# Kernel optimization log

Measured on AMD Instinct MI355X. Metric: run time of the kernel, lower is better.

## Reference

```python
import jax, jax.numpy as jnp
import numpy as np
import math

DIM = 1024
NUM_HEADS = 16
HEAD_DIM = DIM // NUM_HEADS
WINDOW = 256


def setup_inputs() -> dict:
    key = jax.random.key(0)
    k1, k2, k3 = jax.random.split(key, 3)
    B, T = 2, 2048
    x = jax.random.normal(k1, (B, T, DIM), dtype=jnp.float32)
    # nn.Linear weights: [out, in]; y = x @ W.T
    w_qkv = jax.random.normal(k2, (3 * DIM, DIM), dtype=jnp.float32) * (1.0 / math.sqrt(DIM))
    w_out = jax.random.normal(k3, (DIM, DIM), dtype=jnp.float32) * (1.0 / math.sqrt(DIM))
    return {"x": x, "w_qkv": w_qkv, "w_out": w_out}


def _apply_rotary(x, cos, sin):
    # x: [B,H,T,D]; cos/sin: [T, D//2] broadcast over B,H
    d = x.shape[-1] // 2
    x1, x2 = x[..., :d], x[..., d:]
    return jnp.concatenate([x1 * cos - x2 * sin, x2 * cos + x1 * sin], axis=-1)


def reference(x, w_qkv, w_out):
    B, T, C = x.shape
    H, Dh = NUM_HEADS, HEAD_DIM
    qkv = (x @ w_qkv.T).reshape(B, T, 3, H, Dh)
    q, k, v = qkv[:, :, 0], qkv[:, :, 1], qkv[:, :, 2]  # [B,T,H,Dh]
    q = jnp.transpose(q, (0, 2, 1, 3))  # [B,H,T,Dh]
    k = jnp.transpose(k, (0, 2, 1, 3))
    v = jnp.transpose(v, (0, 2, 1, 3))
    # RoPE tables
    inv_freq = 1.0 / (10000.0 ** (jnp.arange(0, Dh, 2, dtype=jnp.float32) / Dh))
    t = jnp.arange(T, dtype=jnp.float32)
    freqs = jnp.einsum('i,j->ij', t, inv_freq)  # [T, Dh//2]
    cos, sin = jnp.cos(freqs), jnp.sin(freqs)
    q = _apply_rotary(q, cos, sin)
    k = _apply_rotary(k, cos, sin)
    scale = 1.0 / math.sqrt(Dh)
    attn = jnp.einsum('bhqd,bhkd->bhqk', q, k) * scale  # [B,H,T,T]
    i = jnp.arange(T)[:, None]
    j = jnp.arange(T)[None, :]
    allowed = (j <= i) & ((i - j) < WINDOW)  # causal + sliding window
    attn = jnp.where(allowed, attn, -jnp.inf)
    attn = jax.nn.softmax(attn, axis=-1)
    out = jnp.einsum('bhqk,bhkd->bhqd', attn, v)
    out = jnp.transpose(out, (0, 2, 1, 3)).reshape(B, T, C)
    return out @ w_out.T
```

## Files before the change

### kernel.cpp

```cpp
#include <hip/hip_runtime.h>
#include <stdint.h>
#include <math.h>

#define T_SEQ 2048
#define NHEAD 16
#define WIN 256

typedef unsigned short u16;
typedef __attribute__((ext_vector_type(8))) short short8;
typedef __attribute__((ext_vector_type(4))) float f32x4;

typedef const __attribute__((address_space(1))) void* gas_ptr;
typedef __attribute__((address_space(3))) void* las_ptr;

__device__ __forceinline__ u16 f2bf(float f) {
  uint32_t u = __builtin_bit_cast(uint32_t, f);
  u += 0x7fffu + ((u >> 16) & 1u);
  return (u16)(u >> 16);
}
__device__ __forceinline__ float bf2f(u16 v) {
  return __builtin_bit_cast(float, ((uint32_t)v) << 16);
}
__device__ __forceinline__ void g2l16(const u16* g, u16* l) {
  __builtin_amdgcn_global_load_lds((gas_ptr)g, (las_ptr)l, 16, 0, 0);
}

__global__ __launch_bounds__(256) void cast_bf16_k(const float* __restrict__ in,
                                                   u16* __restrict__ out, int n4) {
  int i = blockIdx.x * 256 + threadIdx.x;
  if (i >= n4) return;
  const float4 v = reinterpret_cast<const float4*>(in)[i];
  union { u16 h[4]; uint64_t q; } o;
  o.h[0] = f2bf(v.x); o.h[1] = f2bf(v.y); o.h[2] = f2bf(v.z); o.h[3] = f2bf(v.w);
  reinterpret_cast<uint64_t*>(out)[i] = o.q;
}

template <int MODE, typename OUT_T>
__global__ __launch_bounds__(256) void gemm_nt(const u16* __restrict__ A,
                                               const u16* __restrict__ B,
                                               OUT_T* __restrict__ C,
                                               u16* __restrict__ Qb,
                                               u16* __restrict__ Kb,
                                               u16* __restrict__ Vt,
                                               int M, int N, int K) {
  __shared__ u16 lA[3][4096];
  __shared__ u16 lB[3][4096];
  const int tid = threadIdx.x;
  const int lane = tid & 63;
  const int wave = tid >> 6;
  const int r = lane & 15, g = lane >> 4;
  const int wr = wave >> 1, wc = wave & 1;

  const int nbn = N >> 7;
  const int bnpx = nbn >> 3;
  const int bid = blockIdx.x;
  const int xcd = bid & 7, ii = bid >> 3;
  const int bn = xcd * bnpx + (ii % bnpx);
  const int bm = ii / bnpx;

  const u16* Abase = A + (size_t)bm * 128 * K;
  const u16* Bbase = B + (size_t)bn * 128 * K;

  f32x4 acc[4][4];
#pragma unroll
  for (int m = 0; m < 4; m++)
#pragma unroll
    for (int n = 0; n < 4; n++) acc[m][n] = (f32x4){0.f, 0.f, 0.f, 0.f};

  const int c0 = tid, c1 = 256 + tid;
  const int row0 = c0 >> 2, row1 = c1 >> 2;
  const int sw0 = ((c0 & 3) ^ (row0 & 3)) * 8;
  const int sw1 = ((c1 & 3) ^ (row1 & 3)) * 8;
  const int ldsb = wave * 512;

  auto stage = [&](int k0, int b) {
    g2l16(Abase + (size_t)row0 * K + k0 + sw0, &lA[b][ldsb]);
    g2l16(Abase + (size_t)row1 * K + k0 + sw1, &lA[b][2048 + ldsb]);
    g2l16(Bbase + (size_t)row0 * K + k0 + sw0, &lB[b][ldsb]);
    g2l16(Bbase + (size_t)row1 * K + k0 + sw1, &lB[b][2048 + ldsb]);
  };

  const int nt = K >> 5;
  stage(0, 0);
  if (nt > 1) stage(32, 1);
  int cur = 0, pre = 2;

  const int rsw = (r & 3);
  for (int t = 0; t < nt; ++t) {
    if (t + 1 < nt) asm volatile("s_waitcnt vmcnt(4)" ::: "memory");
    else            asm volatile("s_waitcnt vmcnt(0)" ::: "memory");
    __builtin_amdgcn_s_barrier();
    if (t + 2 < nt) stage((t + 2) * 32, pre);

    const u16* la = lA[cur];
    const u16* lb = lB[cur];
    short8 af[4], bfr[4];
#pragma unroll
    for (int m = 0; m < 4; m++)
      af[m] = *reinterpret_cast<const short8*>(
          &la[(wr * 64 + m * 16 + r) * 32 + ((g ^ rsw) * 8)]);
#pragma unroll
    for (int n = 0; n < 4; n++)
      bfr[n] = *reinterpret_cast<const short8*>(
          &lb[(wc * 64 + n * 16 + r) * 32 + ((g ^ rsw) * 8)]);
#pragma unroll
    for (int m = 0; m < 4; m++)
#pragma unroll
      for (int n = 0; n < 4; n++)
        acc[m][n] = __builtin_amdgcn_mfma_f32_16x16x32_bf16(af[m], bfr[n], acc[m][n], 0, 0, 0);
    asm volatile("s_waitcnt lgkmcnt(0)" ::: "memory");
    cur = (cur == 2) ? 0 : cur + 1;
    pre = (pre == 2) ? 0 : pre + 1;
  }

  if constexpr (MODE == 0) {
#pragma unroll
    for (int m = 0; m < 4; m++) {
      const int row = bm * 128 + wr * 64 + m * 16 + g * 4;
#pragma unroll
      for (int n = 0; n < 4; n++) {
        const int col = bn * 128 + wc * 64 + n * 16 + r;
#pragma unroll
        for (int j = 0; j < 4; j++) {
          float v = acc[m][n][j];
          if constexpr (sizeof(OUT_T) == 2)
            C[(size_t)(row + j) * N + col] = f2bf(v);
          else
            C[(size_t)(row + j) * N + col] = v;
        }
      }
    }
  } else {
    const int reg = bn >> 3;
    const int b = bm >> 4;
    const int h = ((bn & 7) << 1) + wc;
    const int bh = b * NHEAD + h;
    const int t0 = ((bm & 15) << 7) + wr * 64;

    if (reg == 2) {
      u16* vb = Vt + (size_t)bh * 64 * T_SEQ;
#pragma unroll
      for (int n = 0; n < 4; n++) {
        const int d = n * 16 + r;
#pragma unroll
        for (int m = 0; m < 4; m++) {
          const int t = t0 + m * 16 + g * 4;
#pragma unroll
          for (int j = 0; j < 4; j++)
            vb[(size_t)d * T_SEQ + t + j] = f2bf(acc[m][n][j]);
        }
      }
    } else {
      u16* qk = (reg == 0 ? Qb : Kb) + (size_t)bh * T_SEQ * 64;
#pragma unroll
      for (int n = 0; n < 2; n++) {
        const int d = n * 16 + r;
        const float inv = exp2f(-(float)d * 0.41524101186092029f);
#pragma unroll
        for (int m = 0; m < 4; m++) {
          const int tb = t0 + m * 16 + g * 4;
#pragma unroll
          for (int j = 0; j < 4; j++) {
            const int t = tb + j;
            float s, c;
            __sincosf((float)t * inv, &s, &c);
            const float x1 = acc[m][n][j], x2 = acc[m][n + 2][j];
            qk[(size_t)t * 64 + d]      = f2bf(x1 * c - x2 * s);
            qk[(size_t)t * 64 + d + 32] = f2bf(x2 * c + x1 * s);
          }
        }
      }
    }
  }
}

__device__ __forceinline__ void stage_kv(const u16* __restrict__ Kh,
                                         const u16* __restrict__ Vh, int k0,
                                         u16* lk, u16* lv, int tid) {
  const int wave = tid >> 6;
#pragma unroll
  for (int p = 0; p < 2; p++) {
    int c = p * 256 + tid;
    int row = c >> 3;
    int col = ((c & 7) ^ (row & 7)) * 8;
    g2l16(Kh + (size_t)(k0 + row) * 64 + col, lk + p * 2048 + wave * 512);
    g2l16(Vh + (size_t)row * T_SEQ + k0 + col, lv + p * 2048 + wave * 512);
  }
}

__global__ __launch_bounds__(256) void attn_k(const u16* __restrict__ Qb,
                                              const u16* __restrict__ Kb,
                                              const u16* __restrict__ Vt,
                                              u16* __restrict__ Ob) {
  const int bid = blockIdx.x;
  const int owned = (bid & 7) * 128 + (bid >> 3);
  const int qt = owned & 31;
  const int bh = owned >> 5;

  const int tid = threadIdx.x, lane = tid & 63, w = tid >> 6;
  const int r = lane & 15, g = lane >> 4;
  const int q0 = qt * 64;
  const u16* Qh = Qb + (size_t)bh * T_SEQ * 64;
  const u16* Kh = Kb + (size_t)bh * T_SEQ * 64;
  const u16* Vh = Vt + (size_t)bh * 64 * T_SEQ;

  __shared__ u16 lK[2][64 * 64];
  __shared__ u16 lV[2][64 * 64];
  __shared__ u16 p_lds[4][16][72];

  short8 aq[2];
#pragma unroll
  for (int kk = 0; kk < 2; kk++)
    aq[kk] = *reinterpret_cast<const short8*>(
        &Qh[(size_t)(q0 + w * 16 + r) * 64 + kk * 32 + g * 8]);

  f32x4 o[4];
#pragma unroll
  for (int n = 0; n < 4; n++) o[n] = (f32x4){0.f, 0.f, 0.f, 0.f};
  float mrun[4], lrun[4];
#pragma unroll
  for (int j = 0; j < 4; j++) { mrun[j] = -1e30f; lrun[j] = 0.f; }

  const int ktlo = (qt >= 4) ? (qt - 4) : 0;
  stage_kv(Kh, Vh, qt * 64, lK[0], lV[0], tid);
  __syncthreads();
  int buf = 0;

  for (int kt = qt; kt >= ktlo; kt--) {
    const int k0 = kt * 64;
    if (kt > ktlo)
      stage_kv(Kh, Vh, (kt - 1) * 64, lK[buf ^ 1], lV[buf ^ 1], tid);

    const u16* lk = lK[buf];
    const u16* lv = lV[buf];
    const int sw = (r & 7) * 8;

    f32x4 s[4];
#pragma unroll
    for (int n = 0; n < 4; n++) {
      f32x4 sn = (f32x4){0.f, 0.f, 0.f, 0.f};
#pragma unroll
      for (int kk = 0; kk < 2; kk++) {
        short8 bk = *reinterpret_cast<const short8*>(
            &lk[(n * 16 + r) * 64 + ((kk * 32 + g * 8) ^ sw)]);
        sn = __builtin_amdgcn_mfma_f32_16x16x32_bf16(aq[kk], bk, sn, 0, 0, 0);
      }
      s[n] = sn;
    }
    float rmax[4] = {-1e30f, -1e30f, -1e30f, -1e30f};
#pragma unroll
    for (int n = 0; n < 4; n++) {
      const int k = k0 + n * 16 + r;
#pragma unroll
      for (int j = 0; j < 4; j++) {
        const int q = q0 + w * 16 + g * 4 + j;
        float v = s[n][j] * 0.125f;
        bool ok = (k <= q) && (q - k < WIN);
        v = ok ? v : -1e30f;
        s[n][j] = v;
        rmax[j] = fmaxf(rmax[j], v);
      }
    }
#pragma unroll
    for (int off = 1; off < 16; off <<= 1)
#pragma unroll
      for (int j = 0; j < 4; j++) rmax[j] = fmaxf(rmax[j], __shfl_xor(rmax[j], off));

    float scl[4];
#pragma unroll
    for (int j = 0; j < 4; j++) {
      float mn = fmaxf(mrun[j], rmax[j]);
      scl[j] = __expf(mrun[j] - mn);
      mrun[j] = mn;
    }
    float rsum[4] = {0.f, 0.f, 0.f, 0.f};
#pragma unroll
    for (int n = 0; n < 4; n++)
#pragma unroll
      for (int j = 0; j < 4; j++) {
        float p = __expf(s[n][j] - mrun[j]);
        s[n][j] = p;
        rsum[j] += p;
      }
#pragma unroll
    for (int off = 1; off < 16; off <<= 1)
#pragma unroll
      for (int j = 0; j < 4; j++) rsum[j] += __shfl_xor(rsum[j], off);
#pragma unroll
    for (int j = 0; j < 4; j++) lrun[j] = lrun[j] * scl[j] + rsum[j];
#pragma unroll
    for (int n = 0; n < 4; n++)
#pragma unroll
      for (int j = 0; j < 4; j++) o[n][j] *= scl[j];

#pragma unroll
    for (int n = 0; n < 4; n++)
#pragma unroll
      for (int j = 0; j < 4; j++) p_lds[w][g * 4 + j][n * 16 + r] = f2bf(s[n][j]);
#pragma unroll
    for (int kk = 0; kk < 2; kk++) {
      short8 ap = *reinterpret_cast<const short8*>(&p_lds[w][r][kk * 32 + g * 8]);
#pragma unroll
      for (int n = 0; n < 4; n++) {
        short8 bv = *reinterpret_cast<const short8*>(
            &lv[(n * 16 + r) * 64 + ((kk * 32 + g * 8) ^ sw)]);
        o[n] = __builtin_amdgcn_mfma_f32_16x16x32_bf16(ap, bv, o[n], 0, 0, 0);
      }
    }
    __syncthreads();
    buf ^= 1;
  }

  const int b = bh >> 4, h = bh & 15;
#pragma unroll
  for (int n = 0; n < 4; n++)
#pragma unroll
    for (int j = 0; j < 4; j++) {
      const int q = q0 + w * 16 + g * 4 + j;
      size_t off = ((size_t)(b * T_SEQ + q)) * 1024 + h * 64 + n * 16 + r;
      Ob[off] = f2bf(o[n][j] / lrun[j]);
    }
}

extern "C" void kernel_launch(void* const* d_in, const int* in_sizes, int n_in,
                              void* d_out, int out_size, void* d_ws, size_t ws_size,
                              hipStream_t stream) {
  const float* x = (const float*)d_in[0];
  const float* w_qkv = (const float*)d_in[1];
  const float* w_out = (const float*)d_in[2];
  float* out = (float*)d_out;
  char* ws = (char*)d_ws;

  u16* xb    = (u16*)(ws + 0);
  u16* wqkvb = (u16*)(ws + 8388608);
  u16* Qb    = (u16*)(ws + 16777216);
  u16* Kb    = (u16*)(ws + 25165824);
  u16* Vt    = (u16*)(ws + 33554432);
  u16* Ob    = (u16*)(ws + 41943040);
  u16* woutb = (u16*)(ws + 50331648);

  cast_bf16_k<<<4096, 256, 0, stream>>>(x, xb, 1048576);
  cast_bf16_k<<<3072, 256, 0, stream>>>(w_qkv, wqkvb, 786432);
  cast_bf16_k<<<1024, 256, 0, stream>>>(w_out, woutb, 262144);

  gemm_nt<1, u16><<<768, 256, 0, stream>>>(xb, wqkvb, (u16*)nullptr,
                                           Qb, Kb, Vt, 4096, 3072, 1024);

  attn_k<<<1024, 256, 0, stream>>>(Qb, Kb, Vt, Ob);

  gemm_nt<0, float><<<256, 256, 0, stream>>>(Ob, woutb, out,
                                             nullptr, nullptr, nullptr,
                                             4096, 1024, 1024);
}
```

Baseline: 171.9 us.

## Use dedicated 256x256-tile QKV GEMM kernel with 4-deep LDS ring

Replaces the templated 128x128 GEMM used for the QKV projection with a dedicated kernel. It uses 256x256 output tiles, 512 threads (8 waves, each computing 128x64), a 4-slot LDS ring with two slices prefetched ahead and a single barrier per K step, and MFMA priority raising. The larger tiles are meant to raise arithmetic intensity and cut redundant global loads. 192 blocks cover the 256 CUs, so some CUs sit idle, and the much larger accumulator raises register pressure. The output-projection GEMM is simplified to an fp32-only path with no behavioural change.

Measured after the change: 182.2 us. +6.0%, slower.

```diff
diff --git a/kernel.cpp b/kernel.cpp
--- a/kernel.cpp
+++ b/kernel.cpp
@@ -35,13 +35,120 @@
   reinterpret_cast<uint64_t*>(out)[i] = o.q;
 }
 
-template <int MODE, typename OUT_T>
+__device__ __forceinline__ void stage_slice(const u16* __restrict__ Ab,
+                                            const u16* __restrict__ Bb,
+                                            int s, u16* la, u16* lb, int tid) {
+  const int w = tid >> 6, l = tid & 63;
+#pragma unroll
+  for (int c = 0; c < 2; c++) {
+    const int rl = c * 128 + w * 16 + (l >> 2);
+    const int sc = ((l & 3) * 8) ^ ((rl & 8) << 1);
+    const size_t so = (size_t)rl * 1024 + s * 32 + sc;
+    g2l16(Ab + so, la + c * 4096 + w * 512);
+    g2l16(Bb + so, lb + c * 4096 + w * 512);
+  }
+}
+
+__global__ __launch_bounds__(512, 1) void gemm256_qkv(const u16* __restrict__ A,
+                                                      const u16* __restrict__ B,
+                                                      u16* __restrict__ Qb,
+                                                      u16* __restrict__ Kb,
+                                                      u16* __restrict__ Vt) {
+  __shared__ u16 ringA[4][8192];
+  __shared__ u16 ringB[4][8192];
+  const int tid = threadIdx.x, lane = tid & 63, wave = tid >> 6;
+  const int r = lane & 15, g = lane >> 4;
+  const int wm = wave >> 2, wn = wave & 3;
+
+  const int flat = (blockIdx.x & 7) * 24 + (blockIdx.x >> 3);
+  const int bn = flat >> 4, bm = flat & 15;
+
+  const u16* Ab = A + (size_t)bm * 256 * 1024;
+  const u16* Bb = B + (size_t)bn * 256 * 1024;
+
+  f32x4 acc[8][4];
+#pragma unroll
+  for (int mi = 0; mi < 8; mi++)
+#pragma unroll
+    for (int ni = 0; ni < 4; ni++) acc[mi][ni] = (f32x4){0.f, 0.f, 0.f, 0.f};
+
+  stage_slice(Ab, Bb, 0, ringA[0], ringB[0], tid);
+  stage_slice(Ab, Bb, 1, ringA[1], ringB[1], tid);
+
+  const int swz = (r & 8) << 1;
+  for (int s = 0; s < 32; ++s) {
+    if (s + 1 < 32) asm volatile("s_waitcnt vmcnt(4)" ::: "memory");
+    else            asm volatile("s_waitcnt vmcnt(0)" ::: "memory");
+    asm volatile("s_barrier" ::: "memory");
+    if (s + 2 < 32)
+      stage_slice(Ab, Bb, s + 2, ringA[(s + 2) & 3], ringB[(s + 2) & 3], tid);
+
+    const u16* la = ringA[s & 3];
+    const u16* lb = ringB[s & 3];
+    short8 af[8], bf[4];
+#pragma unroll
+    for (int mi = 0; mi < 8; mi++)
+      af[mi] = *reinterpret_cast<const short8*>(
+          &la[(wm * 128 + mi * 16 + r) * 32 + ((g * 8) ^ swz)]);
+#pragma unroll
+    for (int ni = 0; ni < 4; ni++)
+      bf[ni] = *reinterpret_cast<const short8*>(
+          &lb[(wn * 64 + ni * 16 + r) * 32 + ((g * 8) ^ swz)]);
+    __builtin_amdgcn_s_setprio(1);
+#pragma unroll
+    for (int mi = 0; mi < 8; mi++)
+#pragma unroll
+      for (int ni = 0; ni < 4; ni++)
+        acc[mi][ni] = __builtin_amdgcn_mfma_f32_16x16x32_bf16(af[mi], bf[ni],
+                                                              acc[mi][ni], 0, 0, 0);
+    __builtin_amdgcn_s_setprio(0);
+  }
+
+  const int reg = bn >> 2;
+  const int b = bm >> 3;
+  const int h = (bn & 3) * 4 + wn;
+  const int bh = b * NHEAD + h;
+  const int t0 = (bm & 7) * 256 + wm * 128;
+
+  if (reg == 2) {
+    u16* vb = Vt + (size_t)bh * 64 * T_SEQ;
+#pragma unroll
+    for (int ni = 0; ni < 4; ni++) {
+      const int d = ni * 16 + r;
+#pragma unroll
+      for (int mi = 0; mi < 8; mi++) {
+        const int t = t0 + mi * 16 + g * 4;
+#pragma unroll
+        for (int j = 0; j < 4; j++)
+          vb[(size_t)d * T_SEQ + t + j] = f2bf(acc[mi][ni][j]);
+      }
+    }
+  } else {
+    u16* qk = (reg == 0 ? Qb : Kb) + (size_t)bh * T_SEQ * 64;
+#pragma unroll
+    for (int ni = 0; ni < 2; ni++) {
+      const int d = ni * 16 + r;
+      const float inv = exp2f(-(float)d * 0.41524101186092029f);
+#pragma unroll
+      for (int mi = 0; mi < 8; mi++) {
+        const int tb = t0 + mi * 16 + g * 4;
+#pragma unroll
+        for (int j = 0; j < 4; j++) {
+          const int t = tb + j;
+          float sn, cs;
+          __sincosf((float)t * inv, &sn, &cs);
+          const float x1 = acc[mi][ni][j], x2 = acc[mi][ni + 2][j];
+          qk[(size_t)t * 64 + d]      = f2bf(x1 * cs - x2 * sn);
+          qk[(size_t)t * 64 + d + 32] = f2bf(x2 * cs + x1 * sn);
+        }
+      }
+    }
+  }
+}
+
 __global__ __launch_bounds__(256) void gemm_nt(const u16* __restrict__ A,
                                                const u16* __restrict__ B,
-                                               OUT_T* __restrict__ C,
-                                               u16* __restrict__ Qb,
-                                               u16* __restrict__ Kb,
-                                               u16* __restrict__ Vt,
+                                               float* __restrict__ C,
                                                int M, int N, int K) {
   __shared__ u16 lA[3][4096];
   __shared__ u16 lB[3][4096];
@@ -113,63 +220,15 @@
     pre = (pre == 2) ? 0 : pre + 1;
   }
 
-  if constexpr (MODE == 0) {
-#pragma unroll
-    for (int m = 0; m < 4; m++) {
-      const int row = bm * 128 + wr * 64 + m * 16 + g * 4;
-#pragma unroll
-      for (int n = 0; n < 4; n++) {
-        const int col = bn * 128 + wc * 64 + n * 16 + r;
-#pragma unroll
-        for (int j = 0; j < 4; j++) {
-          float v = acc[m][n][j];
-          if constexpr (sizeof(OUT_T) == 2)
-            C[(size_t)(row + j) * N + col] = f2bf(v);
-          else
-            C[(size_t)(row + j) * N + col] = v;
-        }
-      }
-    }
-  } else {
-    const int reg = bn >> 3;
-    const int b = bm >> 4;
-    const int h = ((bn & 7) << 1) + wc;
-    const int bh = b * NHEAD + h;
-    const int t0 = ((bm & 15) << 7) + wr * 64;
-
-    if (reg == 2) {
-      u16* vb = Vt + (size_t)bh * 64 * T_SEQ;
-#pragma unroll
-      for (int n = 0; n < 4; n++) {
-        const int d = n * 16 + r;
-#pragma unroll
-        for (int m = 0; m < 4; m++) {
-          const int t = t0 + m * 16 + g * 4;
-#pragma unroll
-          for (int j = 0; j < 4; j++)
-            vb[(size_t)d * T_SEQ + t + j] = f2bf(acc[m][n][j]);
-        }
-      }
-    } else {
-      u16* qk = (reg == 0 ? Qb : Kb) + (size_t)bh * T_SEQ * 64;
-#pragma unroll
-      for (int n = 0; n < 2; n++) {
-        const int d = n * 16 + r;
-        const float inv = exp2f(-(float)d * 0.41524101186092029f);
-#pragma unroll
-        for (int m = 0; m < 4; m++) {
-          const int tb = t0 + m * 16 + g * 4;
-#pragma unroll
-          for (int j = 0; j < 4; j++) {
-            const int t = tb + j;
-            float s, c;
-            __sincosf((float)t * inv, &s, &c);
-            const float x1 = acc[m][n][j], x2 = acc[m][n + 2][j];
-            qk[(size_t)t * 64 + d]      = f2bf(x1 * c - x2 * s);
-            qk[(size_t)t * 64 + d + 32] = f2bf(x2 * c + x1 * s);
-          }
-        }
-      }
+#pragma unroll
+  for (int m = 0; m < 4; m++) {
+    const int row = bm * 128 + wr * 64 + m * 16 + g * 4;
+#pragma unroll
+    for (int n = 0; n < 4; n++) {
+      const int col = bn * 128 + wc * 64 + n * 16 + r;
+#pragma unroll
+      for (int j = 0; j < 4; j++)
+        C[(size_t)(row + j) * N + col] = acc[m][n][j];
     }
   }
 }
@@ -343,12 +402,9 @@
   cast_bf16_k<<<3072, 256, 0, stream>>>(w_qkv, wqkvb, 786432);
   cast_bf16_k<<<1024, 256, 0, stream>>>(w_out, woutb, 262144);
 
-  gemm_nt<1, u16><<<768, 256, 0, stream>>>(xb, wqkvb, (u16*)nullptr,
-                                           Qb, Kb, Vt, 4096, 3072, 1024);
+  gemm256_qkv<<<192, 512, 0, stream>>>(xb, wqkvb, Qb, Kb, Vt);
 
   attn_k<<<1024, 256, 0, stream>>>(Qb, Kb, Vt, Ob);
 
-  gemm_nt<0, float><<<256, 256, 0, stream>>>(Ob, woutb, out,
-                                             nullptr, nullptr, nullptr,
-                                             4096, 1024, 1024);
-}
+  gemm_nt<<<256, 256, 0, stream>>>(Ob, woutb, out, 4096, 1024, 1024);
+}
```
